# Kernel optimization log

Measured on AMD Instinct MI355X. Metric: run time of the kernel, lower is better.

Reference implementation:

```python
import jax, jax.numpy as jnp
import numpy as np

N_NODES = 100000


def gcn_conv(x, W, b, src, dst, n_nodes):
    """PyG GCNConv: D^{-1/2} (A + I) D^{-1/2} X W + b (self loops added)."""
    xw = x @ W  # [N, F_out]
    # degree over A + I, counted on destination (col) side
    deg = jnp.zeros((n_nodes,), dtype=x.dtype).at[dst].add(1.0) + 1.0
    dinv = jax.lax.rsqrt(deg)  # deg >= 1, safe
    # edge messages with symmetric normalization
    coef = dinv[src] * dinv[dst]  # [E]
    msg = xw[src] * coef[:, None]  # [E, F_out]
    agg = jax.ops.segment_sum(msg, dst, num_segments=n_nodes)
    # self-loop contribution: dinv[i]^2 * xw[i]
    out = agg + xw * (dinv * dinv)[:, None]
    return out + b


def setup_inputs() -> dict:
    key = jax.random.key(0)
    k1, k2, k3, k4 = jax.random.split(key, 4)
    input_dim, hidden_dim, output_dim = 64, 64, 32
    n_edges = 1600000
    x = jax.random.normal(k1, (N_NODES, input_dim), dtype=jnp.float32)
    edge_index = jax.random.randint(k2, (2, n_edges), 0, N_NODES, dtype=jnp.int64)
    # Glorot-style init for GCN weights, zero bias (PyG default)
    s1 = (6.0 / (input_dim + hidden_dim)) ** 0.5
    s2 = (6.0 / (hidden_dim + output_dim)) ** 0.5
    W1 = jax.random.uniform(k3, (input_dim, hidden_dim), jnp.float32, -s1, s1)
    W2 = jax.random.uniform(k4, (hidden_dim, output_dim), jnp.float32, -s2, s2)
    b1 = jnp.zeros((hidden_dim,), jnp.float32)
    b2 = jnp.zeros((output_dim,), jnp.float32)
    return {"x": x, "edge_index": edge_index, "W1": W1, "b1": b1, "W2": W2, "b2": b2}


def reference(x, edge_index, W1, b1, W2, b2):
    src, dst = edge_index[0], edge_index[1]
    h = jax.nn.relu(gcn_conv(x, W1, b1, src, dst, N_NODES))
    return gcn_conv(h, W2, b2, src, dst, N_NODES)
```

## Files before the change

### kernel.cpp

```cpp
#include <hip/hip_runtime.h>
#include <hip/hip_fp16.h>

#define NPB2  256
#define K2MAX 400
#define SCAP  4864
#define CCAP2 6656
#define EPBA  2048

typedef _Float16 f16x8 __attribute__((ext_vector_type(8)));
typedef float    f32x4 __attribute__((ext_vector_type(4)));

__global__ __launch_bounds__(256) void sort_pass_a(
    const int* __restrict__ src, const int* __restrict__ dst, int E, int K2,
    int* __restrict__ bin_fill, unsigned* __restrict__ bin_edges) {
    __shared__ int hist[K2MAX];
    __shared__ int lbase[K2MAX];
    __shared__ int gbase[K2MAX];
    __shared__ unsigned sorted[EPBA];
    __shared__ unsigned short sbid[EPBA];
    __shared__ int wsum[4];
    const int t = threadIdx.x;
    for (int i = t; i < K2; i += 256) hist[i] = 0;
    __syncthreads();
    const int e0 = blockIdx.x * EPBA;
    const int m = min(EPBA, E - e0);
    for (int e = t; e < m; e += 256) atomicAdd(&hist[dst[e0 + e] >> 8], 1);
    __syncthreads();
    int i0 = t * 2, i1 = t * 2 + 1;
    int c0 = (i0 < K2) ? hist[i0] : 0;
    int c1 = (i1 < K2) ? hist[i1] : 0;
    int s = c0 + c1;
    int lane = t & 63, w = t >> 6;
    int x = s;
    for (int d = 1; d < 64; d <<= 1) { int y = __shfl_up(x, d, 64); if (lane >= d) x += y; }
    if (lane == 63) wsum[w] = x;
    __syncthreads();
    int run = x - s;
    for (int j = 0; j < 4; ++j) if (j < w) run += wsum[j];
    if (i0 < K2) { lbase[i0] = run; if (c0) gbase[i0] = atomicAdd(&bin_fill[i0], c0); run += c0; }
    if (i1 < K2) { lbase[i1] = run; if (c1) gbase[i1] = atomicAdd(&bin_fill[i1], c1); run += c1; }
    __syncthreads();
    for (int i = t; i < K2; i += 256) hist[i] = 0;
    __syncthreads();
    for (int e = t; e < m; e += 256) {
        int d = dst[e0 + e], b = d >> 8;
        int r = atomicAdd(&hist[b], 1);
        int pos = lbase[b] + r;
        sorted[pos] = ((unsigned)(d & 255) << 17) | (unsigned)src[e0 + e];
        sbid[pos] = (unsigned short)b;
    }
    __syncthreads();
    for (int i = t; i < m; i += 256) {
        int b = sbid[i];
        int off = gbase[b] + (i - lbase[b]);
        if (off < SCAP) bin_edges[(size_t)b * SCAP + off] = sorted[i];
    }
}

__global__ __launch_bounds__(256) void bin_csr(
    const int* __restrict__ bin_fill, const unsigned* __restrict__ bin_edges,
    unsigned* __restrict__ csr, int* __restrict__ rowstart, int* __restrict__ deg,
    float* __restrict__ dinv, int N, unsigned PAD) {
    __shared__ unsigned list[SCAP];
    __shared__ int cnt[NPB2], pref[NPB2], cnt2[NPB2];
    __shared__ int wsum[4];
    const int b = blockIdx.x;
    const int m = min(bin_fill[b], SCAP);
    cnt[threadIdx.x] = 0; cnt2[threadIdx.x] = 0;
    __syncthreads();
    const unsigned* bep = bin_edges + (size_t)b * SCAP;
    for (int e = threadIdx.x; e < m; e += 256) {
        unsigned pk = bep[e];
        list[e] = pk;
        atomicAdd(&cnt[pk >> 17], 1);
    }
    __syncthreads();
    {
        int i = threadIdx.x;
        int c = cnt[i];
        int cpad = (c + 7) & ~7;
        int lane = i & 63, w = i >> 6;
        int x = cpad;
        for (int d = 1; d < 64; d <<= 1) { int y = __shfl_up(x, d, 64); if (lane >= d) x += y; }
        if (lane == 63) wsum[w] = x;
        __syncthreads();
        int ex = x - cpad;
        for (int j = 0; j < 4; ++j) if (j < w) ex += wsum[j];
        pref[i] = ex;
        int g = b * NPB2 + i;
        if (g < N) {
            deg[g] = c;
            rowstart[g] = b * CCAP2 + ex;
            dinv[g] = rsqrtf((float)c + 1.0f);
        }
        for (int p = c; p < cpad; ++p) {
            int ci = ex + p;
            if (ci < CCAP2) csr[(size_t)b * CCAP2 + ci] = PAD;
        }
    }
    __syncthreads();
    for (int e = threadIdx.x; e < m; e += 256) {
        unsigned pk = list[e];
        int dl = pk >> 17;
        int r = atomicAdd(&cnt2[dl], 1);
        int ci = pref[dl] + r;
        if (ci < CCAP2) csr[(size_t)b * CCAP2 + ci] = pk & 0x1FFFF;
    }
}

__global__ void wtrans_k(const float* __restrict__ W1, const float* __restrict__ W2,
                         __half* __restrict__ W1T, __half* __restrict__ W2T) {
    int t = threadIdx.x;
    for (int i = t; i < 64 * 64; i += 256) {
        int f = i >> 6, k = i & 63;
        W1T[i] = __float2half(W1[k * 64 + f]);
    }
    for (int i = t; i < 32 * 64; i += 256) {
        int f = i >> 6, k = i & 63;
        W2T[i] = __float2half(W2[k * 32 + f]);
    }
}

__global__ __launch_bounds__(256) void gemm1_mfma(
    const float* __restrict__ X, const __half* __restrict__ W1T,
    const float* __restrict__ dinv, __half* __restrict__ out, int N) {
    const int wave = threadIdx.x >> 6, lane = threadIdx.x & 63;
    const int r = lane & 15, q = lane >> 4;
    const int nb = blockIdx.x * 64 + wave * 16;
    const int node = min(nb + r, N - 1);
    f32x4 acc[4] = {{0,0,0,0},{0,0,0,0},{0,0,0,0},{0,0,0,0}};
#pragma unroll
    for (int kt = 0; kt < 2; ++kt) {
        const float4* xr = (const float4*)(X + (size_t)node * 64 + kt * 32 + q * 8);
        float4 p0 = xr[0], p1 = xr[1];
        f16x8 a;
        a[0] = (_Float16)p0.x; a[1] = (_Float16)p0.y; a[2] = (_Float16)p0.z; a[3] = (_Float16)p0.w;
        a[4] = (_Float16)p1.x; a[5] = (_Float16)p1.y; a[6] = (_Float16)p1.z; a[7] = (_Float16)p1.w;
#pragma unroll
        for (int c = 0; c < 4; ++c) {
            f16x8 bf = *(const f16x8*)(W1T + (size_t)(c * 16 + r) * 64 + kt * 32 + q * 8);
            acc[c] = __builtin_amdgcn_mfma_f32_16x16x32_f16(a, bf, acc[c], 0, 0, 0);
        }
    }
#pragma unroll
    for (int c = 0; c < 4; ++c)
#pragma unroll
        for (int i = 0; i < 4; ++i) {
            int nd = nb + q * 4 + i;
            if (nd < N) out[(size_t)nd * 64 + c * 16 + r] = __float2half(acc[c][i] * dinv[nd]);
        }
}

__global__ __launch_bounds__(256) void gemm2_mfma(
    const __half* __restrict__ H, const __half* __restrict__ W2T,
    const float* __restrict__ dinv, __half* __restrict__ out, int N) {
    const int wave = threadIdx.x >> 6, lane = threadIdx.x & 63;
    const int r = lane & 15, q = lane >> 4;
    const int nb = blockIdx.x * 64 + wave * 16;
    const int node = min(nb + r, N - 1);
    f32x4 acc[2] = {{0,0,0,0},{0,0,0,0}};
#pragma unroll
    for (int kt = 0; kt < 2; ++kt) {
        f16x8 a = *(const f16x8*)(H + (size_t)node * 64 + kt * 32 + q * 8);
#pragma unroll
        for (int c = 0; c < 2; ++c) {
            f16x8 bf = *(const f16x8*)(W2T + (size_t)(c * 16 + r) * 64 + kt * 32 + q * 8);
            acc[c] = __builtin_amdgcn_mfma_f32_16x16x32_f16(a, bf, acc[c], 0, 0, 0);
        }
    }
#pragma unroll
    for (int c = 0; c < 2; ++c)
#pragma unroll
        for (int i = 0; i < 4; ++i) {
            int nd = nb + q * 4 + i;
            if (nd < N) out[(size_t)nd * 32 + c * 16 + r] = __float2half(acc[c][i] * dinv[nd]);
        }
}

template <int F, bool RELU, bool HOUT>
__global__ __launch_bounds__(256) void aggregate_w(
    const __half* __restrict__ xws, const unsigned* __restrict__ csr,
    const int* __restrict__ rowstart, const int* __restrict__ deg,
    const float* __restrict__ dinv, const float* __restrict__ bias,
    void* __restrict__ outv, int n) {
    constexpr int LPN = F / 8;
    int t = blockIdx.x * 256 + threadIdx.x;
    int node = t / LPN;
    int fl = t - node * LPN;
    if (node >= n) return;
    int mp = (deg[node] + 7) & ~7;
    const unsigned* cp = csr + rowstart[node];
    const float4* tab = (const float4*)xws;
    float4 sv = tab[(size_t)node * LPN + fl];
    float acc[8];
    {
        const __half2* sh = (const __half2*)&sv;
#pragma unroll
        for (int j = 0; j < 4; ++j) { float2 v = __half22float2(sh[j]); acc[2*j] = v.x; acc[2*j+1] = v.y; }
    }
    if (mp > 0) {
        unsigned s[8];
#pragma unroll
        for (int u = 0; u < 8; ++u) s[u] = cp[u];
        for (int e = 8; ; e += 8) {
            float4 d[8];
#pragma unroll
            for (int u = 0; u < 8; ++u) d[u] = tab[(size_t)s[u] * LPN + fl];
            bool more = e < mp;
            unsigned sn[8];
            if (more) {
#pragma unroll
                for (int u = 0; u < 8; ++u) sn[u] = cp[e + u];
            }
#pragma unroll
            for (int u = 0; u < 8; ++u) {
                const __half2* dh = (const __half2*)&d[u];
#pragma unroll
                for (int j = 0; j < 4; ++j) {
                    float2 v = __half22float2(dh[j]);
                    acc[2*j] += v.x; acc[2*j+1] += v.y;
                }
            }
            if (!more) break;
#pragma unroll
            for (int u = 0; u < 8; ++u) s[u] = sn[u];
        }
    }
    float dn = dinv[node];
    float4 b0 = ((const float4*)bias)[fl * 2];
    float4 b1 = ((const float4*)bias)[fl * 2 + 1];
    float bf[8] = {b0.x, b0.y, b0.z, b0.w, b1.x, b1.y, b1.z, b1.w};
    float v[8];
#pragma unroll
    for (int j = 0; j < 8; ++j) {
        v[j] = acc[j] * dn + bf[j];
        if (RELU) v[j] = fmaxf(v[j], 0.f);
    }
    if constexpr (HOUT) {
        __half2 o[4];
#pragma unroll
        for (int j = 0; j < 4; ++j) o[j] = __floats2half2_rn(v[2*j], v[2*j+1]);
        ((float4*)outv)[(size_t)node * LPN + fl] = *(const float4*)o;
    } else {
        float4 o0 = {v[0], v[1], v[2], v[3]};
        float4 o1 = {v[4], v[5], v[6], v[7]};
        float4* op = (float4*)outv + ((size_t)node * F + fl * 8) / 4;
        op[0] = o0; op[1] = o1;
    }
}


extern "C" void kernel_launch(void* const* d_in, const int* in_sizes, int n_in,
                              void* d_out, int out_size, void* d_ws, size_t ws_size,
                              hipStream_t stream) {
    const float* x  = (const float*)d_in[0];
    const int*   ei = (const int*)d_in[1];
    const float* W1 = (const float*)d_in[2];
    const float* b1 = (const float*)d_in[3];
    const float* W2 = (const float*)d_in[4];
    const float* b2 = (const float*)d_in[5];
    float* out = (float*)d_out;

    const int N = in_sizes[0] / 64;
    const int E = in_sizes[1] / 2;
    const int K2 = (N + NPB2 - 1) / NPB2;
    const int* src = ei;
    const int* dst = ei + E;

    unsigned* be    = (unsigned*)d_ws;
    unsigned* csr   = be + (size_t)K2 * SCAP;
    int*      bfill = (int*)(csr + (size_t)K2 * CCAP2);
    int*      rowst = bfill + K2;
    int*      deg   = rowst + N;
    float*    dinv  = (float*)(deg + N);
    __half*   xws   = (__half*)(dinv + N);
    __half*   h     = xws + (size_t)(N + 1) * 64;
    __half*   hw2   = h + (size_t)N * 64;
    __half*   W1T   = hw2 + (size_t)(N + 1) * 32;
    __half*   W2T   = W1T + 64 * 64;

    hipMemsetAsync(bfill, 0, (size_t)K2 * sizeof(int), stream);
    hipMemsetAsync(xws + (size_t)N * 64, 0, 64 * sizeof(__half), stream);
    hipMemsetAsync(hw2 + (size_t)N * 32, 0, 32 * sizeof(__half), stream);

    int ab = (E + EPBA - 1) / EPBA;
    sort_pass_a<<<ab, 256, 0, stream>>>(src, dst, E, K2, bfill, be);
    wtrans_k<<<1, 256, 0, stream>>>(W1, W2, W1T, W2T);
    bin_csr<<<K2, 256, 0, stream>>>(bfill, be, csr, rowst, deg, dinv, N, (unsigned)N);

    int gb = (N + 63) / 64;
    gemm1_mfma<<<gb, 256, 0, stream>>>(x, W1T, dinv, xws, N);
    aggregate_w<64, true, true><<<(N * 8 + 255) / 256, 256, 0, stream>>>(
        xws, csr, rowst, deg, dinv, b1, h, N);
    gemm2_mfma<<<gb, 256, 0, stream>>>(h, W2T, dinv, hw2, N);
    aggregate_w<32, false, false><<<(N * 4 + 255) / 256, 256, 0, stream>>>(
        hw2, csr, rowst, deg, dinv, b2, out, N);
}
```

Baseline: 256.0 us.

## Split layer-1 aggregation into feature halves and merge init work into one kernel

The first-layer neighbor aggregation now runs as two launches, each gathering one 32-feature half of the 64-wide fp16 table. Each pass touches a smaller per-pass working set, which should improve cache hit rates for the random neighbor gathers. The cost is walking the CSR index lists twice. The three memsets and the weight-transpose kernel are merged into a single init kernel, and the edges-per-block count in the sort pass is doubled to cut the block count and raise per-block work.

```diff
diff --git a/kernel.cpp b/kernel.cpp
--- a/kernel.cpp
+++ b/kernel.cpp
@@ -5,10 +5,28 @@
 #define K2MAX 400
 #define SCAP  4864
 #define CCAP2 6656
-#define EPBA  2048
+#define EPBA  4096
 
 typedef _Float16 f16x8 __attribute__((ext_vector_type(8)));
 typedef float    f32x4 __attribute__((ext_vector_type(4)));
+
+__global__ __launch_bounds__(256) void init_k(
+    const float* __restrict__ W1, const float* __restrict__ W2,
+    __half* __restrict__ W1T, __half* __restrict__ W2T,
+    int* __restrict__ bfill, int K2, __half* __restrict__ xws_pad, __half* __restrict__ hw2_pad) {
+    int t = threadIdx.x;
+    for (int i = t; i < 64 * 64; i += 256) {
+        int f = i >> 6, k = i & 63;
+        W1T[i] = __float2half(W1[k * 64 + f]);
+    }
+    for (int i = t; i < 32 * 64; i += 256) {
+        int f = i >> 6, k = i & 63;
+        W2T[i] = __float2half(W2[k * 32 + f]);
+    }
+    for (int i = t; i < K2; i += 256) bfill[i] = 0;
+    if (t < 64) xws_pad[t] = __float2half(0.f);
+    if (t < 32) hw2_pad[t] = __float2half(0.f);
+}
 
 __global__ __launch_bounds__(256) void sort_pass_a(
     const int* __restrict__ src, const int* __restrict__ dst, int E, int K2,
@@ -108,19 +126,6 @@
     }
 }
 
-__global__ void wtrans_k(const float* __restrict__ W1, const float* __restrict__ W2,
-                         __half* __restrict__ W1T, __half* __restrict__ W2T) {
-    int t = threadIdx.x;
-    for (int i = t; i < 64 * 64; i += 256) {
-        int f = i >> 6, k = i & 63;
-        W1T[i] = __float2half(W1[k * 64 + f]);
-    }
-    for (int i = t; i < 32 * 64; i += 256) {
-        int f = i >> 6, k = i & 63;
-        W2T[i] = __float2half(W2[k * 32 + f]);
-    }
-}
-
 __global__ __launch_bounds__(256) void gemm1_mfma(
     const float* __restrict__ X, const __half* __restrict__ W1T,
     const float* __restrict__ dinv, __half* __restrict__ out, int N) {
@@ -177,21 +182,23 @@
         }
 }
 
-template <int F, bool RELU, bool HOUT>
+template <int F, int FH, bool RELU, bool HOUT>
 __global__ __launch_bounds__(256) void aggregate_w(
     const __half* __restrict__ xws, const unsigned* __restrict__ csr,
     const int* __restrict__ rowstart, const int* __restrict__ deg,
     const float* __restrict__ dinv, const float* __restrict__ bias,
-    void* __restrict__ outv, int n) {
-    constexpr int LPN = F / 8;
+    void* __restrict__ outv, int hoff, int n) {
+    constexpr int LPN = FH / 8;
+    constexpr int RS  = F / 8;
     int t = blockIdx.x * 256 + threadIdx.x;
     int node = t / LPN;
     int fl = t - node * LPN;
     if (node >= n) return;
+    int fo = hoff * LPN + fl;
     int mp = (deg[node] + 7) & ~7;
     const unsigned* cp = csr + rowstart[node];
     const float4* tab = (const float4*)xws;
-    float4 sv = tab[(size_t)node * LPN + fl];
+    float4 sv = tab[(size_t)node * RS + fo];
     float acc[8];
     {
         const __half2* sh = (const __half2*)&sv;
@@ -205,7 +212,7 @@
         for (int e = 8; ; e += 8) {
             float4 d[8];
 #pragma unroll
-            for (int u = 0; u < 8; ++u) d[u] = tab[(size_t)s[u] * LPN + fl];
+            for (int u = 0; u < 8; ++u) d[u] = tab[(size_t)s[u] * RS + fo];
             bool more = e < mp;
             unsigned sn[8];
             if (more) {
@@ -227,8 +234,9 @@
         }
     }
     float dn = dinv[node];
-    float4 b0 = ((const float4*)bias)[fl * 2];
-    float4 b1 = ((const float4*)bias)[fl * 2 + 1];
+    const float4* bf4 = (const float4*)bias;
+    float4 b0 = bf4[hoff * (FH / 4) + fl * 2];
+    float4 b1 = bf4[hoff * (FH / 4) + fl * 2 + 1];
     float bf[8] = {b0.x, b0.y, b0.z, b0.w, b1.x, b1.y, b1.z, b1.w};
     float v[8];
 #pragma unroll
@@ -240,11 +248,11 @@
         __half2 o[4];
 #pragma unroll
         for (int j = 0; j < 4; ++j) o[j] = __floats2half2_rn(v[2*j], v[2*j+1]);
-        ((float4*)outv)[(size_t)node * LPN + fl] = *(const float4*)o;
+        ((float4*)outv)[(size_t)node * RS + fo] = *(const float4*)o;
     } else {
         float4 o0 = {v[0], v[1], v[2], v[3]};
         float4 o1 = {v[4], v[5], v[6], v[7]};
-        float4* op = (float4*)outv + ((size_t)node * F + fl * 8) / 4;
+        float4* op = (float4*)outv + (size_t)node * (F / 4) + hoff * (FH / 4) + fl * 2;
         op[0] = o0; op[1] = o1;
     }
 }
@@ -279,20 +287,20 @@
     __half*   W1T   = hw2 + (size_t)(N + 1) * 32;
     __half*   W2T   = W1T + 64 * 64;
 
-    hipMemsetAsync(bfill, 0, (size_t)K2 * sizeof(int), stream);
-    hipMemsetAsync(xws + (size_t)N * 64, 0, 64 * sizeof(__half), stream);
-    hipMemsetAsync(hw2 + (size_t)N * 32, 0, 32 * sizeof(__half), stream);
+    init_k<<<1, 256, 0, stream>>>(W1, W2, W1T, W2T, bfill, K2,
+                                  xws + (size_t)N * 64, hw2 + (size_t)N * 32);
 
     int ab = (E + EPBA - 1) / EPBA;
     sort_pass_a<<<ab, 256, 0, stream>>>(src, dst, E, K2, bfill, be);
-    wtrans_k<<<1, 256, 0, stream>>>(W1, W2, W1T, W2T);
     bin_csr<<<K2, 256, 0, stream>>>(bfill, be, csr, rowst, deg, dinv, N, (unsigned)N);
 
     int gb = (N + 63) / 64;
     gemm1_mfma<<<gb, 256, 0, stream>>>(x, W1T, dinv, xws, N);
-    aggregate_w<64, true, true><<<(N * 8 + 255) / 256, 256, 0, stream>>>(
-        xws, csr, rowst, deg, dinv, b1, h, N);
+    aggregate_w<64, 32, true, true><<<(N * 4 + 255) / 256, 256, 0, stream>>>(
+        xws, csr, rowst, deg, dinv, b1, h, 0, N);
+    aggregate_w<64, 32, true, true><<<(N * 4 + 255) / 256, 256, 0, stream>>>(
+        xws, csr, rowst, deg, dinv, b1, h, 1, N);
     gemm2_mfma<<<gb, 256, 0, stream>>>(h, W2T, dinv, hw2, N);
-    aggregate_w<32, false, false><<<(N * 4 + 255) / 256, 256, 0, stream>>>(
-        hw2, csr, rowst, deg, dinv, b2, out, N);
-}
+    aggregate_w<32, 32, false, false><<<(N * 4 + 255) / 256, 256, 0, stream>>>(
+        hw2, csr, rowst, deg, dinv, b2, out, 0, N);
+}
```

Measured after the change: 260.0 us. About the same (+1.5%).
